# Performance work log

Hardware: AMD Instinct MI355X
Metric: run time of the kernel (lower is better)

## Reference

```python
import jax, jax.numpy as jnp
import numpy as np

B, T, F, H, D1, D2, OUT = 8192, 90, 7, 128, 128, 64, 30


def _layernorm(x, g, b, eps=1e-5):
    mu = jnp.mean(x, axis=-1, keepdims=True)
    var = jnp.mean((x - mu) ** 2, axis=-1, keepdims=True)
    return (x - mu) * jax.lax.rsqrt(var + eps) * g + b


def _lstm_layer(x, Wih, Whh, bih, bhh):
    # x: [B,T,H_in]; Wih: [4H,H_in]; Whh: [4H,H]; biases [4H]. PyTorch gate order i,f,g,o.
    xg = jnp.einsum('bti,gi->btg', x, Wih) + bih + bhh  # [B,T,4H] precomputed input projection
    xg_t = jnp.swapaxes(xg, 0, 1)  # [T,B,4H]

    def step(carry, gx):
        h, c = carry
        gates = gx + h @ Whh.T  # [B,4H]
        i, f, g, o = jnp.split(gates, 4, axis=-1)
        c = jax.nn.sigmoid(f) * c + jax.nn.sigmoid(i) * jnp.tanh(g)
        h = jax.nn.sigmoid(o) * jnp.tanh(c)
        return (h, c), h

    h0 = jnp.zeros((x.shape[0], H), x.dtype)
    (_, _), hs = jax.lax.scan(step, (h0, h0), xg_t)
    return jnp.swapaxes(hs, 0, 1)  # [B,T,H]


def setup_inputs() -> dict:
    key = jax.random.key(0)
    ks = jax.random.split(key, 16)
    s = lambda k, shape, scale: jax.random.normal(k, shape, jnp.float32) * scale
    inp = {
        'x': s(ks[0], (B, T, F), 1.0),
        'W_in': s(ks[1], (H, F), 0.3), 'b_in': jnp.zeros((H,)),
        'g_in': jnp.ones((H,)), 'be_in': jnp.zeros((H,)),
        'Wih0': s(ks[2], (4 * H, H), 0.08), 'Whh0': s(ks[3], (4 * H, H), 0.08),
        'bih0': jnp.zeros((4 * H,)).at[H:2 * H].set(1.0), 'bhh0': jnp.zeros((4 * H,)),
        'Wih1': s(ks[4], (4 * H, H), 0.08), 'Whh1': s(ks[5], (4 * H, H), 0.08),
        'bih1': jnp.zeros((4 * H,)).at[H:2 * H].set(1.0), 'bhh1': jnp.zeros((4 * H,)),
        'g_ln': jnp.ones((H,)), 'be_ln': jnp.zeros((H,)),
        'W_d1': s(ks[6], (D1, H), 0.12), 'b_d1': jnp.zeros((D1,)),
        'W_d2': s(ks[7], (D2, D1), 0.12), 'b_d2': jnp.zeros((D2,)),
        'W_d3': s(ks[8], (OUT, D2), 0.15), 'b_d3': jnp.zeros((OUT,)),
    }
    return inp


def reference(x, W_in, b_in, g_in, be_in,
              Wih0, Whh0, bih0, bhh0, Wih1, Whh1, bih1, bhh1,
              g_ln, be_ln, W_d1, b_d1, W_d2, b_d2, W_d3, b_d3):
    h = _layernorm(jnp.einsum('btf,hf->bth', x, W_in) + b_in, g_in, be_in)
    h = _lstm_layer(h, Wih0, Whh0, bih0, bhh0)
    h = _lstm_layer(h, Wih1, Whh1, bih1, bhh1)  # dropout between layers is eval no-op
    last = _layernorm(h[:, -1, :], g_ln, be_ln)  # [B,H]
    d = jax.nn.relu(last @ W_d1.T + b_d1)
    d = jax.nn.relu(d @ W_d2.T + b_d2)
    return d @ W_d3.T + b_d3  # [B,30]
```

## Files before the change

kernel.cpp:

```cpp
#include <hip/hip_runtime.h>

#define DEV __device__ __forceinline__
typedef unsigned short u16;
typedef unsigned int u32;
typedef __bf16 bf16x8 __attribute__((ext_vector_type(8)));
typedef float f32x4 __attribute__((ext_vector_type(4)));

static constexpr int B = 8192, T = 90, F = 7, H = 128, NOUT = 30;

DEV float fexp2(float x) { return __builtin_amdgcn_exp2f(x); }
DEV float frcp(float x) { return __builtin_amdgcn_rcpf(x); }
DEV float frsq(float x) { return __builtin_amdgcn_rsqf(x); }
DEV float sigm(float x) { return frcp(1.f + fexp2(-1.44269504088896341f * x)); }
DEV u16 f2bfbits(float f) { __bf16 b = (__bf16)f; return __builtin_bit_cast(u16, b); }
DEV float bfbits2f(u32 u) { return __builtin_bit_cast(float, u << 16); }
DEV u32 pk2(float a, float b) { return (u32)f2bfbits(a) | ((u32)f2bfbits(b) << 16); }

DEV float wave_sum(float v) {
#pragma unroll
    for (int m = 32; m; m >>= 1) v += __shfl_xor(v, m, 64);
    return v;
}

__global__ __launch_bounds__(512) void prep_aux(
    const float* __restrict__ W_in, const float* __restrict__ b_in,
    const float* __restrict__ g_in, const float* __restrict__ be_in,
    const float* __restrict__ Wih0, float* __restrict__ aux, u16* __restrict__ Uhat) {
    const int tid = threadIdx.x;
    if (tid < 7) {
        float sm = 0.f, sp = 0.f;
        for (int h = 0; h < 128; ++h) { const float w = W_in[h * 7 + tid]; sm += w; sp += w * b_in[h]; }
        aux[tid] = sm * (1.f / 128.f); aux[64 + tid] = sp * (1.f / 128.f);
    } else if (tid < 56) {
        const int cd = tid - 7, cc = cd / 7, dd = cd % 7;
        float s = 0.f;
        for (int h = 0; h < 128; ++h) s += W_in[h * 7 + cc] * W_in[h * 7 + dd];
        aux[8 + cd] = s * (1.f / 128.f);
    } else if (tid == 56) {
        float s = 0.f; for (int h = 0; h < 128; ++h) s += b_in[h];
        aux[7] = s * (1.f / 128.f);
    } else if (tid == 57) {
        float s = 0.f; for (int h = 0; h < 128; ++h) s += b_in[h] * b_in[h];
        aux[72] = s * (1.f / 128.f);
    }
    float acc[10];
#pragma unroll
    for (int i = 0; i < 10; ++i) acc[i] = 0.f;
    const float* wr = Wih0 + (long)tid * 128;
    for (int h = 0; h < 128; ++h) {
        const float wv = wr[h], wg = wv * g_in[h];
#pragma unroll
        for (int cc = 0; cc < 7; ++cc) acc[cc] += wg * W_in[h * 7 + cc];
        acc[7] += wg * b_in[h]; acc[8] += wg; acc[9] += wv * be_in[h];
    }
    u16* dst = Uhat + tid * 32;
#pragma unroll
    for (int cc = 0; cc < 10; ++cc) dst[cc] = f2bfbits(acc[cc]);
#pragma unroll
    for (int cc = 10; cc < 32; ++cc) dst[cc] = 0;
}

__global__ __launch_bounds__(256) void prep_stats(
    const float* __restrict__ x, const float* __restrict__ aux,
    float2* __restrict__ stats) {
    __shared__ float sa[80];
    const int tid = threadIdx.x;
    if (tid < 80) sa[tid] = aux[tid];
    __syncthreads();
    const long idx = (long)blockIdx.x * 256 + tid;
    const float* xr = x + idx * 7;
    float xv[7];
#pragma unroll
    for (int cc = 0; cc < 7; ++cc) xv[cc] = xr[cc];
    float mu = sa[7];
#pragma unroll
    for (int cc = 0; cc < 7; ++cc) mu += sa[cc] * xv[cc];
    float q = sa[72];
#pragma unroll
    for (int cc = 0; cc < 7; ++cc) {
        float tacc = 2.f * sa[64 + cc];
#pragma unroll
        for (int dd = 0; dd < 7; ++dd) tacc += sa[8 + cc * 7 + dd] * xv[dd];
        q += xv[cc] * tacc;
    }
    const float rstd = frsq(q - mu * mu + 1e-5f);
    stats[idx] = make_float2(rstd, -rstd * mu);
}

#define GATE_R(ACC, CARR, SHROW, R)                                                     \
    {                                                                                   \
        const float xi_ = ACC[0][R] + bias[0];                                          \
        const float xf_ = ACC[1][R] + bias[1];                                          \
        const float xg_ = ACC[2][R] + bias[2];                                          \
        const float xo_ = ACC[3][R] + bias[3];                                          \
        const float tg_ = 2.f * frcp(1.f + fexp2(-2.88539008177792681f * xg_)) - 1.f;   \
        const float cn_ = sigm(xf_) * CARR[R] + sigm(xi_) * tg_;                        \
        CARR[R] = cn_;                                                                  \
        const float so_ = sigm(xo_);                                                    \
        const float rr_ = frcp(1.f + fexp2(-2.88539008177792681f * cn_));               \
        SHROW[hwbase + (R) * 8] = f2bfbits(__builtin_fmaf(2.f * so_, rr_, -so_));       \
    }

__global__ __launch_bounds__(512, 2) void lstm_rec_l1(
    const float* __restrict__ x, const float2* __restrict__ stats,
    const u16* __restrict__ Uhat, const float* __restrict__ Whh,
    const float* __restrict__ bih, const float* __restrict__ bhh,
    u16* __restrict__ hs) {
    __shared__ __align__(16) u16 s_zA[2][4][16][8];
    __shared__ __align__(16) u16 s_zB[2][4][16][8];
    __shared__ __align__(16) u16 s_hA[2][16 * 128];
    __shared__ __align__(16) u16 s_hB[2][16 * 128];

    const int tid = threadIdx.x;
    const int wave = tid >> 6, lane = tid & 63, quad = lane >> 4, n16 = lane & 15;
    const int b0 = blockIdx.x * 32;

    for (int i = tid; i < 2 * 4 * 16 * 8; i += 512) { ((u16*)s_zA)[i] = 0; ((u16*)s_zB)[i] = 0; }
    for (int i = tid; i < 2 * 16 * 128; i += 512) ((u16*)s_hB)[i] = 0;

    bf16x8 bU[4], bWhh[4][4];
    float bias[4];
#pragma unroll
    for (int g = 0; g < 4; ++g) {
        const int wrow = g * 128 + 16 * wave + n16;
        bias[g] = bih[wrow] + bhh[wrow];
        bU[g] = *(const bf16x8*)&Uhat[wrow * 32 + quad * 8];
#pragma unroll
        for (int kk = 0; kk < 4; ++kk) {
            const float* ph = Whh + (long)wrow * 128 + kk * 32 + quad * 8;
            bf16x8 bh;
#pragma unroll
            for (int j = 0; j < 8; ++j) bh[j] = (__bf16)ph[j];
            bWhh[g][kk] = bh;
        }
    }

    const f32x4 zero4 = {0.f, 0.f, 0.f, 0.f};
    float c[2][4];
#pragma unroll
    for (int mt = 0; mt < 2; ++mt)
#pragma unroll
        for (int r = 0; r < 4; ++r) c[mt][r] = 0.f;

    const bool stager = (lane < 8);
    const int tau = wave * 8 + lane;
    const int srow = tau & 31, skk8 = tau >> 5;
    const int smt = srow >> 4, sm = srow & 15;
    const long srowg = (long)(b0 + srow) * T;

    const int ftile = tid >> 8, finner = tid & 255;
    const int fm = finner & 15, fkk8 = finner >> 4;
    const int fldsoff = (fkk8 * 16 + fm) * 8;
    const size_t fgrow = (size_t)(b0 + ftile * 16 + fm) * T;
    const int fgcol = fkk8 * 8;

    const int hwbase = (2 * wave + (n16 >> 3)) * 128 + quad * 32 + (n16 & 7);

    __syncthreads();

    if (stager) {
        const float2 st0 = stats[srowg];
        u32 p0, p1, p2, p3;
        if (skk8 == 0) {
            const float* xp = x + srowg * 7;
            const float rs = st0.x;
            p0 = pk2(rs * xp[0], rs * xp[1]); p1 = pk2(rs * xp[2], rs * xp[3]);
            p2 = pk2(rs * xp[4], rs * xp[5]); p3 = pk2(rs * xp[6], rs);
        } else { p0 = pk2(st0.y, 1.f); p1 = 0; p2 = 0; p3 = 0; }
        *(uint4*)&s_zA[smt][skk8][sm][0] = (uint4){p0, p1, p2, p3};
    }
    __syncthreads();

#define L1_CHAIN_G(AZ, AH, G, OUT)                                                      \
    {                                                                                   \
        f32x4 a_ = __builtin_amdgcn_mfma_f32_16x16x32_bf16(AZ, bU[G], zero4, 0, 0, 0);  \
        a_ = __builtin_amdgcn_mfma_f32_16x16x32_bf16(AH[0], bWhh[G][0], a_, 0, 0, 0);   \
        a_ = __builtin_amdgcn_mfma_f32_16x16x32_bf16(AH[1], bWhh[G][1], a_, 0, 0, 0);   \
        a_ = __builtin_amdgcn_mfma_f32_16x16x32_bf16(AH[2], bWhh[G][2], a_, 0, 0, 0);   \
        a_ = __builtin_amdgcn_mfma_f32_16x16x32_bf16(AH[3], bWhh[G][3], a_, 0, 0, 0);   \
        OUT = a_;                                                                       \
    }

#define L1_STEP(TT, SZR, SZW, SHR, SHW)                                                 \
    {                                                                                   \
        const int t_ = (TT);                                                            \
        const bool hasPre = stager && (t_ + 1 < T);                                     \
        float2 nst = {};                                                                \
        float nx[7];                                                                    \
        if (hasPre) {                                                                   \
            nst = stats[srowg + t_ + 1];                                                \
            if (skk8 == 0) {                                                            \
                const float* xp = x + (srowg + t_ + 1) * 7;                             \
                _Pragma("unroll") for (int j = 0; j < 7; ++j) nx[j] = xp[j];            \
            }                                                                           \
        }                                                                               \
        if (t_ > 0) {                       \
            const uint4 hv_ = *(const uint4*)&SHR[ftile][fldsoff];                      \
            *(uint4*)(hs + (fgrow + (t_ - 1)) * 128 + fgcol) = hv_;                     \
        }                                                                               \
        bf16x8 az0, ah0[4];                                                             \
        az0 = *(const bf16x8*)&SZR[0][quad][n16][0];                                    \
        _Pragma("unroll") for (int kk = 0; kk < 4; ++kk)                                \
            ah0[kk] = *(const bf16x8*)&SHR[0][(kk * 4 + quad) * 128 + n16 * 8];         \
        f32x4 acc0[4], acc1[4];                                                         \
        L1_CHAIN_G(az0, ah0, 0, acc0[0])                                                \
        L1_CHAIN_G(az0, ah0, 1, acc0[1])                                                \
        L1_CHAIN_G(az0, ah0, 2, acc0[2])                                                \
        L1_CHAIN_G(az0, ah0, 3, acc0[3])                                                \
        bf16x8 az1, ah1[4];                                                             \
        az1 = *(const bf16x8*)&SZR[1][quad][n16][0];                                    \
        _Pragma("unroll") for (int kk = 0; kk < 4; ++kk)                                \
            ah1[kk] = *(const bf16x8*)&SHR[1][(kk * 4 + quad) * 128 + n16 * 8];         \
        L1_CHAIN_G(az1, ah1, 0, acc1[0])                                                \
        GATE_R(acc0, c[0], SHW[0], 0)                                                   \
        L1_CHAIN_G(az1, ah1, 1, acc1[1])                                                \
        GATE_R(acc0, c[0], SHW[0], 1)                                                   \
        L1_CHAIN_G(az1, ah1, 2, acc1[2])                                                \
        GATE_R(acc0, c[0], SHW[0], 2)                                                   \
        L1_CHAIN_G(az1, ah1, 3, acc1[3])                                                \
        GATE_R(acc0, c[0], SHW[0], 3)                                                   \
        GATE_R(acc1, c[1], SHW[1], 0)                                                   \
        GATE_R(acc1, c[1], SHW[1], 1)                                                   \
        GATE_R(acc1, c[1], SHW[1], 2)                                                   \
        GATE_R(acc1, c[1], SHW[1], 3)                                                   \
        if (hasPre) {                                                \
            u32 p0_, p1_, p2_, p3_;                                                     \
            if (skk8 == 0) {                                                            \
                const float rs_ = nst.x;                                                \
                p0_ = pk2(rs_ * nx[0], rs_ * nx[1]); p1_ = pk2(rs_ * nx[2], rs_ * nx[3]); \
                p2_ = pk2(rs_ * nx[4], rs_ * nx[5]); p3_ = pk2(rs_ * nx[6], rs_);       \
            } else { p0_ = pk2(nst.y, 1.f); p1_ = 0; p2_ = 0; p3_ = 0; }                \
            *(uint4*)&SZW[smt][skk8][sm][0] = (uint4){p0_, p1_, p2_, p3_};              \
        }                                                                               \
        __syncthreads();                                                                \
    }

#pragma unroll 1
    for (int t = 0; t < T; t += 2) {
        L1_STEP(t, s_zA, s_zB, s_hB, s_hA)
        L1_STEP(t + 1, s_zB, s_zA, s_hA, s_hB)
    }
#undef L1_STEP
#undef L1_CHAIN_G
    {
        const uint4 hv = *(const uint4*)&s_hB[ftile][fldsoff];
        *(uint4*)(hs + (fgrow + (T - 1)) * 128 + fgcol) = hv;
    }
}

__global__ __launch_bounds__(512, 2) void lstm_rec_l2(
    const float* __restrict__ Wih, const float* __restrict__ Whh,
    const float* __restrict__ bih, const float* __restrict__ bhh,
    const u16* __restrict__ xin, u16* __restrict__ hlast) {
    __shared__ __align__(16) u16 s_xA[2][16 * 128];
    __shared__ __align__(16) u16 s_xB[2][16 * 128];
    __shared__ __align__(16) u16 s_hA[2][16 * 128];
    __shared__ __align__(16) u16 s_hB[2][16 * 128];

    const int tid = threadIdx.x;
    const int wave = tid >> 6, lane = tid & 63, quad = lane >> 4, n16 = lane & 15;
    const int b0 = blockIdx.x * 32;

    for (int i = tid; i < 2 * 16 * 128; i += 512) ((u16*)s_hB)[i] = 0;

    bf16x8 bWih[4][4], bWhh[4][4];
    float bias[4];
#pragma unroll
    for (int g = 0; g < 4; ++g) {
        const int wrow = g * 128 + 16 * wave + n16;
        bias[g] = bih[wrow] + bhh[wrow];
#pragma unroll
        for (int kk = 0; kk < 4; ++kk) {
            const float* pi = Wih + (long)wrow * 128 + kk * 32 + quad * 8;
            const float* ph = Whh + (long)wrow * 128 + kk * 32 + quad * 8;
            bf16x8 bi, bh;
#pragma unroll
            for (int j = 0; j < 8; ++j) { bi[j] = (__bf16)pi[j]; bh[j] = (__bf16)ph[j]; }
            bWih[g][kk] = bi; bWhh[g][kk] = bh;
        }
    }

    const f32x4 zero4 = {0.f, 0.f, 0.f, 0.f};
    float c[2][4];
#pragma unroll
    for (int mt = 0; mt < 2; ++mt)
#pragma unroll
        for (int r = 0; r < 4; ++r) c[mt][r] = 0.f;

    const int stile = tid >> 8, sinner = tid & 255;
    const int sm = sinner & 15, skk8 = sinner >> 4;
    const u16* gsrc = xin + (size_t)(b0 + stile * 16 + sm) * T * 128 + skk8 * 8;
    const int ftile = tid >> 8, finner = tid & 255;
    const int fm = finner & 15, fkk8 = finner >> 4;
    const int fldsoff = (fkk8 * 16 + fm) * 8;
    const int fgcol = fkk8 * 8;

    const int hwbase = (2 * wave + (n16 >> 3)) * 128 + quad * 32 + (n16 & 7);

    {
        const uint4 v = *(const uint4*)gsrc;
        *(uint4*)&s_xA[stile][sinner * 8] = v;
    }
    __syncthreads();

#define L2_CHAIN_G(ALN, AH, G, OUT)                                                     \
    {                                                                                   \
        f32x4 a_ = __builtin_amdgcn_mfma_f32_16x16x32_bf16(ALN[0], bWih[G][0], zero4, 0, 0, 0); \
        a_ = __builtin_amdgcn_mfma_f32_16x16x32_bf16(AH[0], bWhh[G][0], a_, 0, 0, 0);   \
        a_ = __builtin_amdgcn_mfma_f32_16x16x32_bf16(ALN[1], bWih[G][1], a_, 0, 0, 0);  \
        a_ = __builtin_amdgcn_mfma_f32_16x16x32_bf16(AH[1], bWhh[G][1], a_, 0, 0, 0);   \
        a_ = __builtin_amdgcn_mfma_f32_16x16x32_bf16(ALN[2], bWih[G][2], a_, 0, 0, 0);  \
        a_ = __builtin_amdgcn_mfma_f32_16x16x32_bf16(AH[2], bWhh[G][2], a_, 0, 0, 0);   \
        a_ = __builtin_amdgcn_mfma_f32_16x16x32_bf16(ALN[3], bWih[G][3], a_, 0, 0, 0);  \
        a_ = __builtin_amdgcn_mfma_f32_16x16x32_bf16(AH[3], bWhh[G][3], a_, 0, 0, 0);   \
        OUT = a_;                                                                       \
    }

#define L2_STEP(TT, SXR, SXW, SHR, SHW)                                                 \
    {                                                                                   \
        const int t_ = (TT);                                                            \
        const bool hasPre = (t_ + 1 < T);                                               \
        uint4 pre = {};                                                                 \
        if (hasPre) pre = *(const uint4*)(gsrc + (size_t)(t_ + 1) * 128);               \
        bf16x8 aln0[4], ah0[4];                                                         \
        _Pragma("unroll") for (int kk = 0; kk < 4; ++kk) {                              \
            const int ro = (kk * 4 + quad) * 128 + n16 * 8;                             \
            aln0[kk] = *(const bf16x8*)&SXR[0][ro];                                     \
            ah0[kk] = *(const bf16x8*)&SHR[0][ro];                                      \
        }                                                                               \
        f32x4 acc0[4], acc1[4];                                                         \
        L2_CHAIN_G(aln0, ah0, 0, acc0[0])                                               \
        L2_CHAIN_G(aln0, ah0, 1, acc0[1])                                               \
        L2_CHAIN_G(aln0, ah0, 2, acc0[2])                                               \
        L2_CHAIN_G(aln0, ah0, 3, acc0[3])                                               \
        bf16x8 aln1[4], ah1[4];                                                         \
        _Pragma("unroll") for (int kk = 0; kk < 4; ++kk) {                              \
            const int ro = (kk * 4 + quad) * 128 + n16 * 8;                             \
            aln1[kk] = *(const bf16x8*)&SXR[1][ro];                                     \
            ah1[kk] = *(const bf16x8*)&SHR[1][ro];                                      \
        }                                                                               \
        L2_CHAIN_G(aln1, ah1, 0, acc1[0])                                               \
        GATE_R(acc0, c[0], SHW[0], 0)                                                   \
        L2_CHAIN_G(aln1, ah1, 1, acc1[1])                                               \
        GATE_R(acc0, c[0], SHW[0], 1)                                                   \
        L2_CHAIN_G(aln1, ah1, 2, acc1[2])                                               \
        GATE_R(acc0, c[0], SHW[0], 2)                                                   \
        L2_CHAIN_G(aln1, ah1, 3, acc1[3])                                               \
        GATE_R(acc0, c[0], SHW[0], 3)                                                   \
        GATE_R(acc1, c[1], SHW[1], 0)                                                   \
        GATE_R(acc1, c[1], SHW[1], 1)                                                   \
        GATE_R(acc1, c[1], SHW[1], 2)                                                   \
        GATE_R(acc1, c[1], SHW[1], 3)                                                   \
        if (hasPre) *(uint4*)&SXW[stile][sinner * 8] = pre;                             \
        __syncthreads();                                                                \
    }

#pragma unroll 1
    for (int t = 0; t < T; t += 2) {
        L2_STEP(t, s_xA, s_xB, s_hB, s_hA)
        L2_STEP(t + 1, s_xB, s_xA, s_hA, s_hB)
    }
#undef L2_STEP
#undef L2_CHAIN_G
    {
        const uint4 hv = *(const uint4*)&s_hB[ftile][fldsoff];
        *(uint4*)(hlast + (size_t)(b0 + ftile * 16 + fm) * 128 + fgcol) = hv;
    }
}

__global__ __launch_bounds__(256) void dense_head(
    const u16* __restrict__ hlast, const float* __restrict__ g_ln,
    const float* __restrict__ be_ln, const float* __restrict__ W_d1,
    const float* __restrict__ b_d1, const float* __restrict__ W_d2,
    const float* __restrict__ b_d2, const float* __restrict__ W_d3,
    const float* __restrict__ b_d3, float* __restrict__ out) {
    __shared__ float s_ln[16][128];
    __shared__ float s_d1[16][128];
    __shared__ float s_d2[16][64];
    const int wave = threadIdx.x >> 6, lane = threadIdx.x & 63;
    const long base = (long)blockIdx.x * 16;
    const int R = wave * 4;

#pragma unroll
    for (int rr = 0; rr < 4; ++rr) {
        const long row = base + R + rr;
        const u32 packed = ((const u32*)hlast)[row * 64 + lane];
        float v0 = bfbits2f(packed & 0xffffu), v1 = bfbits2f(packed >> 16);
        const float s = wave_sum(v0 + v1);
        const float q = wave_sum(v0 * v0 + v1 * v1);
        const float mu = s * (1.f / 128.f);
        const float rstd = frsq(q * (1.f / 128.f) - mu * mu + 1e-5f);
        const int h0 = 2 * lane;
        s_ln[R + rr][h0] = (v0 - mu) * rstd * g_ln[h0] + be_ln[h0];
        s_ln[R + rr][h0 + 1] = (v1 - mu) * rstd * g_ln[h0 + 1] + be_ln[h0 + 1];
    }
    __syncthreads();

#pragma unroll
    for (int half = 0; half < 2; ++half) {
        const int o = lane + 64 * half;
        float a[4] = {b_d1[o], b_d1[o], b_d1[o], b_d1[o]};
        const float4* wr = (const float4*)(W_d1 + (long)o * 128);
#pragma unroll 8
        for (int k = 0; k < 32; ++k) {
            const float4 wv = wr[k];
#pragma unroll
            for (int rr = 0; rr < 4; ++rr) {
                const float4 xv = ((const float4*)s_ln[R + rr])[k];
                a[rr] += wv.x * xv.x + wv.y * xv.y + wv.z * xv.z + wv.w * xv.w;
            }
        }
#pragma unroll
        for (int rr = 0; rr < 4; ++rr) s_d1[R + rr][o] = fmaxf(a[rr], 0.f);
    }
    __syncthreads();

    {
        float a[4] = {b_d2[lane], b_d2[lane], b_d2[lane], b_d2[lane]};
        const float4* wr = (const float4*)(W_d2 + (long)lane * 128);
#pragma unroll 8
        for (int k = 0; k < 32; ++k) {
            const float4 wv = wr[k];
#pragma unroll
            for (int rr = 0; rr < 4; ++rr) {
                const float4 xv = ((const float4*)s_d1[R + rr])[k];
                a[rr] += wv.x * xv.x + wv.y * xv.y + wv.z * xv.z + wv.w * xv.w;
            }
        }
#pragma unroll
        for (int rr = 0; rr < 4; ++rr) s_d2[R + rr][lane] = fmaxf(a[rr], 0.f);
    }
    __syncthreads();

    if (lane < NOUT) {
        float a[4] = {b_d3[lane], b_d3[lane], b_d3[lane], b_d3[lane]};
        const float4* wr = (const float4*)(W_d3 + (long)lane * 64);
#pragma unroll
        for (int k = 0; k < 16; ++k) {
            const float4 wv = wr[k];
#pragma unroll
            for (int rr = 0; rr < 4; ++rr) {
                const float4 xv = ((const float4*)s_d2[R + rr])[k];
                a[rr] += wv.x * xv.x + wv.y * xv.y + wv.z * xv.z + wv.w * xv.w;
            }
        }
#pragma unroll
        for (int rr = 0; rr < 4; ++rr) out[(base + R + rr) * NOUT + lane] = a[rr];
    }
}

extern "C" void kernel_launch(void* const* d_in, const int* in_sizes, int n_in,
                              void* d_out, int out_size, void* d_ws, size_t ws_size,
                              hipStream_t stream) {
    const float* x = (const float*)d_in[0];
    const float* W_in = (const float*)d_in[1];
    const float* b_in = (const float*)d_in[2];
    const float* g_in = (const float*)d_in[3];
    const float* be_in = (const float*)d_in[4];
    const float* Wih0 = (const float*)d_in[5];
    const float* Whh0 = (const float*)d_in[6];
    const float* bih0 = (const float*)d_in[7];
    const float* bhh0 = (const float*)d_in[8];
    const float* Wih1 = (const float*)d_in[9];
    const float* Whh1 = (const float*)d_in[10];
    const float* bih1 = (const float*)d_in[11];
    const float* bhh1 = (const float*)d_in[12];
    const float* g_ln = (const float*)d_in[13];
    const float* be_ln = (const float*)d_in[14];
    const float* W_d1 = (const float*)d_in[15];
    const float* b_d1 = (const float*)d_in[16];
    const float* W_d2 = (const float*)d_in[17];
    const float* b_d2 = (const float*)d_in[18];
    const float* W_d3 = (const float*)d_in[19];
    const float* b_d3 = (const float*)d_in[20];
    float* out = (float*)d_out;

    char* w = (char*)d_ws;
    float* aux = (float*)w;               w += 512;
    u16* Uhat = (u16*)w;                  w += 512 * 32 * sizeof(u16);
    float2* stats = (float2*)w;           w += (size_t)B * T * sizeof(float2);
    u16* hs0 = (u16*)w;                   w += (size_t)B * T * H * sizeof(u16);
    u16* hlast = (u16*)w;

    prep_aux<<<1, 512, 0, stream>>>(W_in, b_in, g_in, be_in, Wih0, aux, Uhat);
    prep_stats<<<(B * T) / 256, 256, 0, stream>>>(x, aux, stats);
    lstm_rec_l1<<<B / 32, 512, 0, stream>>>(x, stats, Uhat, Whh0, bih0, bhh0, hs0);
    lstm_rec_l2<<<B / 32, 512, 0, stream>>>(Wih1, Whh1, bih1, bhh1, hs0, hlast);
    dense_head<<<B / 16, 256, 0, stream>>>(hlast, g_ln, be_ln, W_d1, b_d1, W_d2, b_d2,
                                           W_d3, b_d3, out);
}
```

Before: 533.8 us.

## Software-pipeline LSTM recurrence across the two batch tiles with half-step barriers

Restructures both recurrent LSTM kernels so the MFMA chain for one 16-row batch tile overlaps the gate nonlinearities of the other tile. The schedule becomes half-steps, each followed by a barrier, with prologue and epilogue blocks. The intent is to hide the transcendental gate latency behind matrix-core work, at the cost of twice as many __syncthreads per timestep and more live accumulator registers. The hidden-state flush to global memory is also split per tile and spread across the half-steps.

```diff
diff --git a/kernel.cpp b/kernel.cpp
--- a/kernel.cpp
+++ b/kernel.cpp
@@ -136,6 +136,7 @@
     }
 
     const f32x4 zero4 = {0.f, 0.f, 0.f, 0.f};
+    f32x4 accA[4], accB[4];
     float c[2][4];
 #pragma unroll
     for (int mt = 0; mt < 2; ++mt)
@@ -148,10 +149,8 @@
     const int smt = srow >> 4, sm = srow & 15;
     const long srowg = (long)(b0 + srow) * T;
 
-    const int ftile = tid >> 8, finner = tid & 255;
-    const int fm = finner & 15, fkk8 = finner >> 4;
+    const int fm = tid & 15, fkk8 = (tid >> 4) & 15;
     const int fldsoff = (fkk8 * 16 + fm) * 8;
-    const size_t fgrow = (size_t)(b0 + ftile * 16 + fm) * T;
     const int fgcol = fkk8 * 8;
 
     const int hwbase = (2 * wave + (n16 >> 3)) * 128 + quad * 32 + (n16 & 7);
@@ -171,7 +170,7 @@
     }
     __syncthreads();
 
-#define L1_CHAIN_G(AZ, AH, G, OUT)                                                      \
+#define L1_CH(AZ, AH, G, OUT)                                                           \
     {                                                                                   \
         f32x4 a_ = __builtin_amdgcn_mfma_f32_16x16x32_bf16(AZ, bU[G], zero4, 0, 0, 0);  \
         a_ = __builtin_amdgcn_mfma_f32_16x16x32_bf16(AH[0], bWhh[G][0], a_, 0, 0, 0);   \
@@ -181,71 +180,125 @@
         OUT = a_;                                                                       \
     }
 
-#define L1_STEP(TT, SZR, SZW, SHR, SHW)                                                 \
-    {                                                                                   \
-        const int t_ = (TT);                                                            \
-        const bool hasPre = stager && (t_ + 1 < T);                                     \
-        float2 nst = {};                                                                \
-        float nx[7];                                                                    \
-        if (hasPre) {                                                                   \
-            nst = stats[srowg + t_ + 1];                                                \
-            if (skk8 == 0) {                                                            \
-                const float* xp = x + (srowg + t_ + 1) * 7;                             \
-                _Pragma("unroll") for (int j = 0; j < 7; ++j) nx[j] = xp[j];            \
-            }                                                                           \
+#define L1_BODY(MT, SZ, SHR, ACCN, GT, ACCP, SHW)                                       \
+    {                                                                                   \
+        const bf16x8 az_ = *(const bf16x8*)&SZ[MT][quad][n16][0];                       \
+        bf16x8 ah_[4];                                                                  \
+        _Pragma("unroll") for (int kk = 0; kk < 4; ++kk)                                \
+            ah_[kk] = *(const bf16x8*)&SHR[MT][((kk * 4 + quad) * 16 + n16) * 8];       \
+        L1_CH(az_, ah_, 0, ACCN[0]) GATE_R(ACCP, c[GT], SHW[GT], 0)                     \
+        L1_CH(az_, ah_, 1, ACCN[1]) GATE_R(ACCP, c[GT], SHW[GT], 1)                     \
+        L1_CH(az_, ah_, 2, ACCN[2]) GATE_R(ACCP, c[GT], SHW[GT], 2)                     \
+        L1_CH(az_, ah_, 3, ACCN[3]) GATE_R(ACCP, c[GT], SHW[GT], 3)                     \
+    }
+
+#define L1_BODY_NOG(MT, SZ, SHR, ACCN)                                                  \
+    {                                                                                   \
+        const bf16x8 az_ = *(const bf16x8*)&SZ[MT][quad][n16][0];                       \
+        bf16x8 ah_[4];                                                                  \
+        _Pragma("unroll") for (int kk = 0; kk < 4; ++kk)                                \
+            ah_[kk] = *(const bf16x8*)&SHR[MT][((kk * 4 + quad) * 16 + n16) * 8];       \
+        L1_CH(az_, ah_, 0, ACCN[0])                                                     \
+        L1_CH(az_, ah_, 1, ACCN[1])                                                     \
+        L1_CH(az_, ah_, 2, ACCN[2])                                                     \
+        L1_CH(az_, ah_, 3, ACCN[3])                                                     \
+    }
+
+#define L1_FLUSH(FT, TFL, SHF)                                                          \
+    if (tid < 256) {                                                                    \
+        const uint4 hv_ = *(const uint4*)&SHF[FT][fldsoff];                             \
+        *(uint4*)(hs + ((size_t)(b0 + (FT) * 16 + fm) * T + (TFL)) * 128 + fgcol) = hv_; \
+    }
+
+#define L1_STAGE_LOAD(TN)                                                               \
+    float2 nst_ = {}; float nx_[7];                                                     \
+    if (stager) {                                                                       \
+        nst_ = stats[srowg + (TN)];                                                     \
+        if (skk8 == 0) {                                                                \
+            const float* xp_ = x + (srowg + (TN)) * 7;                                  \
+            _Pragma("unroll") for (int j = 0; j < 7; ++j) nx_[j] = xp_[j];              \
         }                                                                               \
-        if (t_ > 0) {                       \
-            const uint4 hv_ = *(const uint4*)&SHR[ftile][fldsoff];                      \
-            *(uint4*)(hs + (fgrow + (t_ - 1)) * 128 + fgcol) = hv_;                     \
-        }                                                                               \
-        bf16x8 az0, ah0[4];                                                             \
-        az0 = *(const bf16x8*)&SZR[0][quad][n16][0];                                    \
-        _Pragma("unroll") for (int kk = 0; kk < 4; ++kk)                                \
-            ah0[kk] = *(const bf16x8*)&SHR[0][(kk * 4 + quad) * 128 + n16 * 8];         \
-        f32x4 acc0[4], acc1[4];                                                         \
-        L1_CHAIN_G(az0, ah0, 0, acc0[0])                                                \
-        L1_CHAIN_G(az0, ah0, 1, acc0[1])                                                \
-        L1_CHAIN_G(az0, ah0, 2, acc0[2])                                                \
-        L1_CHAIN_G(az0, ah0, 3, acc0[3])                                                \
-        bf16x8 az1, ah1[4];                                                             \
-        az1 = *(const bf16x8*)&SZR[1][quad][n16][0];                                    \
-        _Pragma("unroll") for (int kk = 0; kk < 4; ++kk)                                \
-            ah1[kk] = *(const bf16x8*)&SHR[1][(kk * 4 + quad) * 128 + n16 * 8];         \
-        L1_CHAIN_G(az1, ah1, 0, acc1[0])                                                \
-        GATE_R(acc0, c[0], SHW[0], 0)                                                   \
-        L1_CHAIN_G(az1, ah1, 1, acc1[1])                                                \
-        GATE_R(acc0, c[0], SHW[0], 1)                                                   \
-        L1_CHAIN_G(az1, ah1, 2, acc1[2])                                                \
-        GATE_R(acc0, c[0], SHW[0], 2)                                                   \
-        L1_CHAIN_G(az1, ah1, 3, acc1[3])                                                \
-        GATE_R(acc0, c[0], SHW[0], 3)                                                   \
-        GATE_R(acc1, c[1], SHW[1], 0)                                                   \
-        GATE_R(acc1, c[1], SHW[1], 1)                                                   \
-        GATE_R(acc1, c[1], SHW[1], 2)                                                   \
-        GATE_R(acc1, c[1], SHW[1], 3)                                                   \
-        if (hasPre) {                                                \
-            u32 p0_, p1_, p2_, p3_;                                                     \
-            if (skk8 == 0) {                                                            \
-                const float rs_ = nst.x;                                                \
-                p0_ = pk2(rs_ * nx[0], rs_ * nx[1]); p1_ = pk2(rs_ * nx[2], rs_ * nx[3]); \
-                p2_ = pk2(rs_ * nx[4], rs_ * nx[5]); p3_ = pk2(rs_ * nx[6], rs_);       \
-            } else { p0_ = pk2(nst.y, 1.f); p1_ = 0; p2_ = 0; p3_ = 0; }                \
-            *(uint4*)&SZW[smt][skk8][sm][0] = (uint4){p0_, p1_, p2_, p3_};              \
-        }                                                                               \
-        __syncthreads();                                                                \
+    }
+
+#define L1_STAGE_COMMIT(SZW)                                                            \
+    if (stager) {                                                                       \
+        u32 p0_, p1_, p2_, p3_;                                                         \
+        if (skk8 == 0) {                                                                \
+            const float rs_ = nst_.x;                                                   \
+            p0_ = pk2(rs_ * nx_[0], rs_ * nx_[1]); p1_ = pk2(rs_ * nx_[2], rs_ * nx_[3]); \
+            p2_ = pk2(rs_ * nx_[4], rs_ * nx_[5]); p3_ = pk2(rs_ * nx_[6], rs_);        \
+        } else { p0_ = pk2(nst_.y, 1.f); p1_ = 0; p2_ = 0; p3_ = 0; }                   \
+        *(uint4*)&SZW[smt][skk8][sm][0] = (uint4){p0_, p1_, p2_, p3_};                  \
+    }
+
+    {
+        L1_STAGE_LOAD(1)
+        L1_BODY_NOG(0, s_zA, s_hB, accA)
+        L1_STAGE_COMMIT(s_zB)
+        __syncthreads();
     }
 
 #pragma unroll 1
-    for (int t = 0; t < T; t += 2) {
-        L1_STEP(t, s_zA, s_zB, s_hB, s_hA)
-        L1_STEP(t + 1, s_zB, s_zA, s_hA, s_hB)
-    }
-#undef L1_STEP
-#undef L1_CHAIN_G
-    {
-        const uint4 hv = *(const uint4*)&s_hB[ftile][fldsoff];
-        *(uint4*)(hs + (fgrow + (T - 1)) * 128 + fgcol) = hv;
-    }
+    for (int t = 0; t < 88; t += 2) {
+        {
+            if (t > 0) L1_FLUSH(1, t - 1, s_hB)
+            L1_BODY(1, s_zA, s_hB, accB, 0, accA, s_hA)
+            __syncthreads();
+        }
+        {
+            L1_STAGE_LOAD(t + 2)
+            L1_FLUSH(0, t, s_hA)
+            L1_BODY(0, s_zB, s_hA, accA, 1, accB, s_hA)
+            L1_STAGE_COMMIT(s_zA)
+            __syncthreads();
+        }
+        {
+            L1_FLUSH(1, t, s_hA)
+            L1_BODY(1, s_zB, s_hA, accB, 0, accA, s_hB)
+            __syncthreads();
+        }
+        {
+            L1_STAGE_LOAD(t + 3)
+            L1_FLUSH(0, t + 1, s_hB)
+            L1_BODY(0, s_zA, s_hB, accA, 1, accB, s_hB)
+            L1_STAGE_COMMIT(s_zB)
+            __syncthreads();
+        }
+    }
+    {
+        L1_FLUSH(1, 87, s_hB)
+        L1_BODY(1, s_zA, s_hB, accB, 0, accA, s_hA)
+        __syncthreads();
+    }
+    {
+        L1_FLUSH(0, 88, s_hA)
+        L1_BODY(0, s_zB, s_hA, accA, 1, accB, s_hA)
+        __syncthreads();
+    }
+    {
+        L1_FLUSH(1, 88, s_hA)
+        L1_BODY(1, s_zB, s_hA, accB, 0, accA, s_hB)
+        __syncthreads();
+    }
+    {
+        GATE_R(accB, c[1], s_hB[1], 0)
+        GATE_R(accB, c[1], s_hB[1], 1)
+        GATE_R(accB, c[1], s_hB[1], 2)
+        GATE_R(accB, c[1], s_hB[1], 3)
+        __syncthreads();
+    }
+    {
+        const int ftile = tid >> 8, finner = tid & 255;
+        const int efm = finner & 15, efkk8 = finner >> 4;
+        const uint4 hv = *(const uint4*)&s_hB[ftile][(efkk8 * 16 + efm) * 8];
+        *(uint4*)(hs + ((size_t)(b0 + ftile * 16 + efm) * T + (T - 1)) * 128 + efkk8 * 8) = hv;
+    }
+#undef L1_CH
+#undef L1_BODY
+#undef L1_BODY_NOG
+#undef L1_FLUSH
+#undef L1_STAGE_LOAD
+#undef L1_STAGE_COMMIT
 }
 
 __global__ __launch_bounds__(512, 2) void lstm_rec_l2(
@@ -281,6 +334,7 @@
     }
 
     const f32x4 zero4 = {0.f, 0.f, 0.f, 0.f};
+    f32x4 accA[4], accB[4];
     float c[2][4];
 #pragma unroll
     for (int mt = 0; mt < 2; ++mt)
@@ -288,84 +342,115 @@
         for (int r = 0; r < 4; ++r) c[mt][r] = 0.f;
 
     const int stile = tid >> 8, sinner = tid & 255;
-    const int sm = sinner & 15, skk8 = sinner >> 4;
-    const u16* gsrc = xin + (size_t)(b0 + stile * 16 + sm) * T * 128 + skk8 * 8;
-    const int ftile = tid >> 8, finner = tid & 255;
-    const int fm = finner & 15, fkk8 = finner >> 4;
-    const int fldsoff = (fkk8 * 16 + fm) * 8;
-    const int fgcol = fkk8 * 8;
+    const int ssm = sinner & 15, sskk8 = sinner >> 4;
+    const u16* gsrc = xin + (size_t)(b0 + stile * 16 + ssm) * T * 128 + sskk8 * 8;
+    const int soff = sinner * 8;
 
     const int hwbase = (2 * wave + (n16 >> 3)) * 128 + quad * 32 + (n16 & 7);
 
     {
         const uint4 v = *(const uint4*)gsrc;
-        *(uint4*)&s_xA[stile][sinner * 8] = v;
-    }
-    __syncthreads();
-
-#define L2_CHAIN_G(ALN, AH, G, OUT)                                                     \
-    {                                                                                   \
-        f32x4 a_ = __builtin_amdgcn_mfma_f32_16x16x32_bf16(ALN[0], bWih[G][0], zero4, 0, 0, 0); \
+        *(uint4*)&s_xA[stile][soff] = v;
+    }
+    __syncthreads();
+
+#define L2_CH(AX, AH, G, OUT)                                                           \
+    {                                                                                   \
+        f32x4 a_ = __builtin_amdgcn_mfma_f32_16x16x32_bf16(AX[0], bWih[G][0], zero4, 0, 0, 0); \
         a_ = __builtin_amdgcn_mfma_f32_16x16x32_bf16(AH[0], bWhh[G][0], a_, 0, 0, 0);   \
-        a_ = __builtin_amdgcn_mfma_f32_16x16x32_bf16(ALN[1], bWih[G][1], a_, 0, 0, 0);  \
+        a_ = __builtin_amdgcn_mfma_f32_16x16x32_bf16(AX[1], bWih[G][1], a_, 0, 0, 0);   \
         a_ = __builtin_amdgcn_mfma_f32_16x16x32_bf16(AH[1], bWhh[G][1], a_, 0, 0, 0);   \
-        a_ = __builtin_amdgcn_mfma_f32_16x16x32_bf16(ALN[2], bWih[G][2], a_, 0, 0, 0);  \
+        a_ = __builtin_amdgcn_mfma_f32_16x16x32_bf16(AX[2], bWih[G][2], a_, 0, 0, 0);   \
         a_ = __builtin_amdgcn_mfma_f32_16x16x32_bf16(AH[2], bWhh[G][2], a_, 0, 0, 0);   \
-        a_ = __builtin_amdgcn_mfma_f32_16x16x32_bf16(ALN[3], bWih[G][3], a_, 0, 0, 0);  \
+        a_ = __builtin_amdgcn_mfma_f32_16x16x32_bf16(AX[3], bWih[G][3], a_, 0, 0, 0);   \
         a_ = __builtin_amdgcn_mfma_f32_16x16x32_bf16(AH[3], bWhh[G][3], a_, 0, 0, 0);   \
         OUT = a_;                                                                       \
     }
 
-#define L2_STEP(TT, SXR, SXW, SHR, SHW)                                                 \
-    {                                                                                   \
-        const int t_ = (TT);                                                            \
-        const bool hasPre = (t_ + 1 < T);                                               \
-        uint4 pre = {};                                                                 \
-        if (hasPre) pre = *(const uint4*)(gsrc + (size_t)(t_ + 1) * 128);               \
-        bf16x8 aln0[4], ah0[4];                                                         \
+#define L2_BODY(MT, SX, SHR, ACCN, GT, ACCP, SHW)                                       \
+    {                                                                                   \
+        bf16x8 ax_[4], ah_[4];                                                          \
         _Pragma("unroll") for (int kk = 0; kk < 4; ++kk) {                              \
-            const int ro = (kk * 4 + quad) * 128 + n16 * 8;                             \
-            aln0[kk] = *(const bf16x8*)&SXR[0][ro];                                     \
-            ah0[kk] = *(const bf16x8*)&SHR[0][ro];                                      \
+            const int ro_ = ((kk * 4 + quad) * 16 + n16) * 8;                           \
+            ax_[kk] = *(const bf16x8*)&SX[MT][ro_];                                     \
+            ah_[kk] = *(const bf16x8*)&SHR[MT][ro_];                                    \
         }                                                                               \
-        f32x4 acc0[4], acc1[4];                                                         \
-        L2_CHAIN_G(aln0, ah0, 0, acc0[0])                                               \
-        L2_CHAIN_G(aln0, ah0, 1, acc0[1])                                               \
-        L2_CHAIN_G(aln0, ah0, 2, acc0[2])                                               \
-        L2_CHAIN_G(aln0, ah0, 3, acc0[3])                                               \
-        bf16x8 aln1[4], ah1[4];                                                         \
+        L2_CH(ax_, ah_, 0, ACCN[0]) GATE_R(ACCP, c[GT], SHW[GT], 0)                     \
+        L2_CH(ax_, ah_, 1, ACCN[1]) GATE_R(ACCP, c[GT], SHW[GT], 1)                     \
+        L2_CH(ax_, ah_, 2, ACCN[2]) GATE_R(ACCP, c[GT], SHW[GT], 2)                     \
+        L2_CH(ax_, ah_, 3, ACCN[3]) GATE_R(ACCP, c[GT], SHW[GT], 3)                     \
+    }
+
+#define L2_BODY_NOG(MT, SX, SHR, ACCN)                                                  \
+    {                                                                                   \
+        bf16x8 ax_[4], ah_[4];                                                          \
         _Pragma("unroll") for (int kk = 0; kk < 4; ++kk) {                              \
-            const int ro = (kk * 4 + quad) * 128 + n16 * 8;                             \
-            aln1[kk] = *(const bf16x8*)&SXR[1][ro];                                     \
-            ah1[kk] = *(const bf16x8*)&SHR[1][ro];                                      \
+            const int ro_ = ((kk * 4 + quad) * 16 + n16) * 8;                           \
+            ax_[kk] = *(const bf16x8*)&SX[MT][ro_];                                     \
+            ah_[kk] = *(const bf16x8*)&SHR[MT][ro_];                                    \
         }                                                                               \
-        L2_CHAIN_G(aln1, ah1, 0, acc1[0])                                               \
-        GATE_R(acc0, c[0], SHW[0], 0)                                                   \
-        L2_CHAIN_G(aln1, ah1, 1, acc1[1])                                               \
-        GATE_R(acc0, c[0], SHW[0], 1)                                                   \
-        L2_CHAIN_G(aln1, ah1, 2, acc1[2])                                               \
-        GATE_R(acc0, c[0], SHW[0], 2)                                                   \
-        L2_CHAIN_G(aln1, ah1, 3, acc1[3])                                               \
-        GATE_R(acc0, c[0], SHW[0], 3)                                                   \
-        GATE_R(acc1, c[1], SHW[1], 0)                                                   \
-        GATE_R(acc1, c[1], SHW[1], 1)                                                   \
-        GATE_R(acc1, c[1], SHW[1], 2)                                                   \
-        GATE_R(acc1, c[1], SHW[1], 3)                                                   \
-        if (hasPre) *(uint4*)&SXW[stile][sinner * 8] = pre;                             \
-        __syncthreads();                                                                \
+        L2_CH(ax_, ah_, 0, ACCN[0])                                                     \
+        L2_CH(ax_, ah_, 1, ACCN[1])                                                     \
+        L2_CH(ax_, ah_, 2, ACCN[2])                                                     \
+        L2_CH(ax_, ah_, 3, ACCN[3])                                                     \
+    }
+
+    {
+        const uint4 pre_ = *(const uint4*)(gsrc + 128);
+        L2_BODY_NOG(0, s_xA, s_hB, accA)
+        *(uint4*)&s_xB[stile][soff] = pre_;
+        __syncthreads();
     }
 
 #pragma unroll 1
-    for (int t = 0; t < T; t += 2) {
-        L2_STEP(t, s_xA, s_xB, s_hB, s_hA)
-        L2_STEP(t + 1, s_xB, s_xA, s_hA, s_hB)
-    }
-#undef L2_STEP
-#undef L2_CHAIN_G
-    {
-        const uint4 hv = *(const uint4*)&s_hB[ftile][fldsoff];
-        *(uint4*)(hlast + (size_t)(b0 + ftile * 16 + fm) * 128 + fgcol) = hv;
-    }
+    for (int t = 0; t < 88; t += 2) {
+        {
+            L2_BODY(1, s_xA, s_hB, accB, 0, accA, s_hA)
+            __syncthreads();
+        }
+        {
+            const uint4 pre_ = *(const uint4*)(gsrc + (size_t)(t + 2) * 128);
+            L2_BODY(0, s_xB, s_hA, accA, 1, accB, s_hA)
+            *(uint4*)&s_xA[stile][soff] = pre_;
+            __syncthreads();
+        }
+        {
+            L2_BODY(1, s_xB, s_hA, accB, 0, accA, s_hB)
+            __syncthreads();
+        }
+        {
+            const uint4 pre_ = *(const uint4*)(gsrc + (size_t)(t + 3) * 128);
+            L2_BODY(0, s_xA, s_hB, accA, 1, accB, s_hB)
+            *(uint4*)&s_xB[stile][soff] = pre_;
+            __syncthreads();
+        }
+    }
+    {
+        L2_BODY(1, s_xA, s_hB, accB, 0, accA, s_hA)
+        __syncthreads();
+    }
+    {
+        L2_BODY(0, s_xB, s_hA, accA, 1, accB, s_hA)
+        __syncthreads();
+    }
+    {
+        L2_BODY(1, s_xB, s_hA, accB, 0, accA, s_hB)
+        __syncthreads();
+    }
+    {
+        GATE_R(accB, c[1], s_hB[1], 0)
+        GATE_R(accB, c[1], s_hB[1], 1)
+        GATE_R(accB, c[1], s_hB[1], 2)
+        GATE_R(accB, c[1], s_hB[1], 3)
+        __syncthreads();
+    }
+    {
+        const uint4 hv = *(const uint4*)&s_hB[stile][soff];
+        *(uint4*)(hlast + (size_t)(b0 + stile * 16 + ssm) * 128 + sskk8 * 8) = hv;
+    }
+#undef L2_CH
+#undef L2_BODY
+#undef L2_BODY_NOG
 }
 
 __global__ __launch_bounds__(256) void dense_head(
```

New measurement: 535.9 us. About the same (+0.4%).
